# Optimization experiments

Hardware: AMD Instinct MI355X
Metric: run time of the kernel (lower is better)

## Reference

```python
import jax, jax.numpy as jnp
import numpy as np

N = 32768       # total nodes across the batch of graphs
E = 524288      # total edges
D = 512         # feature dim (dimensions = [512, 512, 512])
G = 512         # number of graphs (64 nodes each)


def setup_inputs() -> dict:
    key = jax.random.key(0)
    ks = jax.random.split(key, 16)
    inp = {
        'feat': jax.random.normal(ks[0], (N, D), jnp.float32),
        'src': jax.random.randint(ks[1], (E,), 0, N, jnp.int32),
        'dst': jax.random.randint(ks[2], (E,), 0, N, jnp.int32),
        'adj_vals': jax.random.uniform(ks[3], (E,), jnp.float32),
        'graph_ids': (jnp.arange(N, dtype=jnp.int32) // (N // G)),
        'W0': jax.random.normal(ks[4], (D, D), jnp.float32) * 0.05,
        'b0': jnp.zeros((D,), jnp.float32),
        'W1': jax.random.normal(ks[5], (D, D), jnp.float32) * 0.05,
        'b1': jnp.zeros((D,), jnp.float32),
        'gW1': jax.random.normal(ks[6], (D, D), jnp.float32) * 0.05,
        'gb1': jnp.zeros((D,), jnp.float32),
        'gW2': jax.random.normal(ks[7], (D, D), jnp.float32) * 0.05,
        'gb2': jnp.zeros((D,), jnp.float32),
        'gW3': jax.random.normal(ks[8], (D, D), jnp.float32) * 0.05,
        'gb3': jnp.zeros((D,), jnp.float32),
        'gWs': jax.random.normal(ks[9], (D, D), jnp.float32) * 0.05,
        'gbs': jnp.zeros((D,), jnp.float32),
    }
    return inp


def reference(feat, src, dst, adj_vals, graph_ids,
              W0, b0, W1, b1,
              gW1, gb1, gW2, gb2, gW3, gb3, gWs, gbs):
    # GCN layer: act(A_hat @ (X W) + b), A_hat given as weighted edge list
    def gcn(h, W, b, act):
        support = h @ W                              # [N, D]
        msg = adj_vals[:, None] * support[src]       # [E, D]
        agg = jax.ops.segment_sum(msg, dst, num_segments=N)
        return act(agg + b)

    h = gcn(feat, W0, b0, jax.nn.relu)               # hidden layer, act=relu
    h = gcn(h, W1, b1, lambda x: x)                  # last layer, identity act

    # pooling: per-graph mean readout -> sigmoid -> repeat-expand back to nodes
    ones = jnp.ones((N, 1), h.dtype)
    counts = jax.ops.segment_sum(ones, graph_ids, num_segments=G)   # [G, 1]
    pooled = jax.ops.segment_sum(h, graph_ids, num_segments=G) / counts
    g = jax.nn.sigmoid(pooled)[graph_ids]            # [N, D] repeat-expanded

    z = jax.nn.relu(g @ gW1 + gb1)
    z = jax.nn.relu(z @ gW2 + gb2)
    z = jax.nn.relu(z @ gW3 + gb3)
    return z + (g @ gWs + gbs)
```

## Files before the change

### kernel.cpp

```cpp
#include <hip/hip_runtime.h>

typedef unsigned int u32;
typedef unsigned short u16;

typedef __attribute__((ext_vector_type(8))) __bf16 bf16x8;
typedef __attribute__((ext_vector_type(4))) float f32x4;
typedef __attribute__((ext_vector_type(2))) float f32x2;
typedef __attribute__((ext_vector_type(4))) u32 u32x4;

#define N_NODES 32768
#define N_EDGES 524288
#define DIM 512
#define N_GRAPHS 512
#define ECAP 1536
#define NB_CONV 8192
#define NB_TR 1536

__device__ __forceinline__ u16 f2b(float f) {
  union { float f; u32 u; } v; v.f = f;
  u32 r = v.u + 0x7FFFu + ((v.u >> 16) & 1u);
  return (u16)(r >> 16);
}
__device__ __forceinline__ u32 pack2(float a, float b) {
  return (u32)f2b(a) | ((u32)f2b(b) << 16);
}
__device__ __forceinline__ float blo(u32 u) { union { u32 u; float f; } v; v.u = u << 16; return v.f; }
__device__ __forceinline__ float bhi(u32 u) { union { u32 u; float f; } v; v.u = u & 0xFFFF0000u; return v.f; }
__device__ __forceinline__ float b2f(u16 u) { union { u32 u; float f; } v; v.u = ((u32)u) << 16; return v.f; }

__device__ __forceinline__ void async16(const void* g, void* l) {
  __builtin_amdgcn_global_load_lds(
      (const __attribute__((address_space(1))) u32*)g,
      (__attribute__((address_space(3))) u32*)l, 16, 0, 0);
}

__device__ __forceinline__ void acc8(f32x2* a, u32x4 raw, float v) {
  f32x2 v2 = {v, v};
  a[0] += v2 * f32x2{blo(raw.x), bhi(raw.x)};
  a[1] += v2 * f32x2{blo(raw.y), bhi(raw.y)};
  a[2] += v2 * f32x2{blo(raw.z), bhi(raw.z)};
  a[3] += v2 * f32x2{blo(raw.w), bhi(raw.w)};
}

struct WPack {
  const float* src[6];
  u16* dst[6];
};
__global__ __launch_bounds__(256)
void k_prep(const float* __restrict__ feat, u16* __restrict__ featb, WPack wp,
            const int* __restrict__ dstv, int* __restrict__ counts) {
  __shared__ float tile[32][33];
  const int bid = blockIdx.x, tid = threadIdx.x;
  if (bid < NB_CONV) {
    int i = bid * 256 + tid;
    const float4* p = (const float4*)feat;
    float4 a = p[2 * i], b = p[2 * i + 1];
    uint4 o;
    o.x = pack2(a.x, a.y); o.y = pack2(a.z, a.w);
    o.z = pack2(b.x, b.y); o.w = pack2(b.z, b.w);
    ((uint4*)featb)[i] = o;
  } else if (bid < NB_CONV + NB_TR) {
    int idx = bid - NB_CONV;
    int bz = idx >> 8, rem = idx & 255, by = rem >> 4, bx = rem & 15;
    const float* W = wp.src[bz];
    u16* Wt = wp.dst[bz];
    int tx = tid & 31, ty = tid >> 5;
    int bx32 = bx * 32, by32 = by * 32;
    #pragma unroll
    for (int i = 0; i < 4; i++)
      tile[ty + 8 * i][tx] = W[(size_t)(by32 + ty + 8 * i) * DIM + bx32 + tx];
    __syncthreads();
    #pragma unroll
    for (int i = 0; i < 4; i++)
      Wt[(size_t)(bx32 + ty + 8 * i) * DIM + by32 + tx] = f2b(tile[tx][ty + 8 * i]);
  } else {
    int i = (bid - NB_CONV - NB_TR) * 256 + tid;
    atomicAdd(&counts[dstv[i]], 1);
  }
}

__global__ void k_scan(const int* __restrict__ counts, int* __restrict__ offsets,
                       int* __restrict__ cursor) {
  __shared__ int part[1024];
  int t = threadIdx.x;
  const int4* c4 = (const int4*)counts;
  int4 cv[8];
  #pragma unroll
  for (int j = 0; j < 8; j++) cv[j] = c4[t * 8 + j];
  int loc[32];
  int s = 0;
  #pragma unroll
  for (int j = 0; j < 8; j++) {
    loc[4 * j + 0] = s; s += cv[j].x;
    loc[4 * j + 1] = s; s += cv[j].y;
    loc[4 * j + 2] = s; s += cv[j].z;
    loc[4 * j + 3] = s; s += cv[j].w;
  }
  part[t] = s;
  __syncthreads();
  for (int off = 1; off < 1024; off <<= 1) {
    int v = (t >= off) ? part[t - off] : 0;
    __syncthreads();
    part[t] += v;
    __syncthreads();
  }
  int excl = (t == 0) ? 0 : part[t - 1];
  #pragma unroll
  for (int j = 0; j < 8; j++) {
    int4 o = make_int4(excl + loc[4 * j], excl + loc[4 * j + 1],
                       excl + loc[4 * j + 2], excl + loc[4 * j + 3]);
    ((int4*)offsets)[t * 8 + j] = o;
    ((int4*)cursor)[t * 8 + j] = o;
  }
  if (t == 1023) offsets[N_NODES] = excl + s;
}

__global__ void k_fill(const int* __restrict__ src, const int* __restrict__ dst,
                       const float* __restrict__ vals, int* __restrict__ cursor,
                       int2* __restrict__ epack) {
  int i = blockIdx.x * 256 + threadIdx.x;
  if (i >= N_EDGES) return;
  int d = dst[i];
  int p = atomicAdd(&cursor[d], 1);
  epack[p] = make_int2(src[i], __float_as_int(vals[i]));
}

__global__ __launch_bounds__(256)
void k_gemm_bt(const u16* __restrict__ A, const u16* __restrict__ Bt,
               u16* __restrict__ Cout, int M, int Nout, int K) {
  __shared__ __align__(16) u16 As[128 * 32];
  __shared__ __align__(16) u16 Bs[128 * 32];
  const int tid = threadIdx.x;
  const int l = tid & 63;
  const int w = tid >> 6;
  const int mBase = blockIdx.x * 128;
  const int nBase = blockIdx.y * 128;
  const int wm = (w >> 1) * 64;
  const int wn = (w & 1) * 64;
  const int lrow = l >> 2;
  const int lcol = (l & 3) * 8;
  const int q = l >> 4;
  const int r = l & 15;
  f32x4 acc[4][4] = {};

  for (int k0 = 0; k0 < K; k0 += 32) {
    #pragma unroll
    for (int p = 0; p < 2; p++) {
      int row = w * 32 + p * 16 + lrow;
      async16(A + (size_t)(mBase + row) * K + k0 + lcol, (char*)As + w * 2048 + p * 1024);
      async16(Bt + (size_t)(nBase + row) * K + k0 + lcol, (char*)Bs + w * 2048 + p * 1024);
    }
    __syncthreads();
    bf16x8 af[4], bfr[4];
    #pragma unroll
    for (int i = 0; i < 4; i++) af[i] = *(const bf16x8*)&As[(wm + i * 16 + r) * 32 + q * 8];
    #pragma unroll
    for (int j = 0; j < 4; j++) bfr[j] = *(const bf16x8*)&Bs[(wn + j * 16 + r) * 32 + q * 8];
    #pragma unroll
    for (int i = 0; i < 4; i++)
      #pragma unroll
      for (int j = 0; j < 4; j++)
        acc[i][j] = __builtin_amdgcn_mfma_f32_16x16x32_bf16(af[i], bfr[j], acc[i][j], 0, 0, 0);
    __syncthreads();
  }

  #pragma unroll
  for (int i = 0; i < 4; i++) {
    #pragma unroll
    for (int j = 0; j < 4; j++) {
      int col = nBase + wn + j * 16 + r;
      #pragma unroll
      for (int reg = 0; reg < 4; reg++) {
        int rowg = mBase + wm + i * 16 + q * 4 + reg;
        Cout[(size_t)rowg * Nout + col] = f2b(acc[i][j][reg]);
      }
    }
  }
}

template <bool RELU, bool ADDEND, bool OUTF32, bool SIGMOID>
__global__ __launch_bounds__(256)
void k_gemm_small(const u16* __restrict__ A, const u16* __restrict__ Bt,
                  const float* __restrict__ bias, const u16* __restrict__ addend,
                  void* __restrict__ Cout, int Nout, int K) {
  __shared__ __align__(16) u16 As[64 * 32];
  __shared__ __align__(16) u16 Bs[64 * 32];
  const int tid = threadIdx.x;
  const int l = tid & 63;
  const int w = tid >> 6;
  const int mBase = blockIdx.x * 64;
  const int nBase = blockIdx.y * 64;
  const int wm = (w >> 1) * 32;
  const int wn = (w & 1) * 32;
  const int lrow = tid >> 2;
  const int lcol = (tid & 3) * 8;
  const int q = l >> 4;
  const int r = l & 15;
  f32x4 acc[2][2] = {};

  for (int k0 = 0; k0 < K; k0 += 32) {
    async16(A + (size_t)(mBase + lrow) * K + k0 + lcol, (char*)As + tid * 16);
    async16(Bt + (size_t)(nBase + lrow) * K + k0 + lcol, (char*)Bs + tid * 16);
    __syncthreads();
    bf16x8 af[2], bfr[2];
    #pragma unroll
    for (int i = 0; i < 2; i++) af[i] = *(const bf16x8*)&As[(wm + i * 16 + r) * 32 + q * 8];
    #pragma unroll
    for (int j = 0; j < 2; j++) bfr[j] = *(const bf16x8*)&Bs[(wn + j * 16 + r) * 32 + q * 8];
    #pragma unroll
    for (int i = 0; i < 2; i++)
      #pragma unroll
      for (int j = 0; j < 2; j++)
        acc[i][j] = __builtin_amdgcn_mfma_f32_16x16x32_bf16(af[i], bfr[j], acc[i][j], 0, 0, 0);
    __syncthreads();
  }

  #pragma unroll
  for (int i = 0; i < 2; i++) {
    #pragma unroll
    for (int j = 0; j < 2; j++) {
      int col = nBase + wn + j * 16 + r;
      float bv = bias[col];
      #pragma unroll
      for (int reg = 0; reg < 4; reg++) {
        int rowg = mBase + wm + i * 16 + q * 4 + reg;
        float v = acc[i][j][reg] + bv;
        if (ADDEND) v += b2f(addend[(size_t)rowg * Nout + col]);
        if (RELU) v = fmaxf(v, 0.0f);
        if (SIGMOID) v = 1.0f / (1.0f + expf(-v));
        if (OUTF32) ((float*)Cout)[(size_t)rowg * Nout + col] = v;
        else ((u16*)Cout)[(size_t)rowg * Nout + col] = f2b(v);
      }
    }
  }
}

template <bool RELU, bool POOL>
__global__ __launch_bounds__(256)
void k_agg(const u16* __restrict__ support, const int* __restrict__ offsets,
           const int2* __restrict__ epack, const float* __restrict__ bias,
           u16* __restrict__ outp) {
  __shared__ int2 eLds[ECAP];
  __shared__ float poolLds[4][64];
  const int chunk = blockIdx.x & 7;
  const int cidx  = blockIdx.x >> 3;
  const int rowBase = cidx * 64;
  const int e0b = offsets[rowBase];
  const int nb = offsets[rowBase + 64] - e0b;
  for (int i = threadIdx.x; i < min(nb, ECAP); i += 256)
    eLds[i] = epack[e0b + i];
  __syncthreads();

  const int wi = threadIdx.x >> 6;
  const int l  = threadIdx.x & 63;
  const int grp = l >> 3;
  const int li  = l & 7;
  const int colOff = chunk * 64 + li * 8;
  const u16* spc = support + colOff;

  f32x2 b[4] = {};
  if (!POOL) {
    const float4* bp = (const float4*)(bias + colOff);
    float4 x = bp[0], y = bp[1];
    b[0] = f32x2{x.x, x.y}; b[1] = f32x2{x.z, x.w};
    b[2] = f32x2{y.x, y.y}; b[3] = f32x2{y.z, y.w};
  }

  f32x2 psum[4] = {};

  #pragma unroll
  for (int pass = 0; pass < 2; pass++) {
    int r = rowBase + wi * 16 + pass * 8 + grp;
    int re0 = offsets[r] - e0b;
    int deg = offsets[r + 1] - e0b - re0;

    f32x2 a[4] = {b[0], b[1], b[2], b[3]};

    if (nb <= ECAP) {
      int i = 0;
      for (; i + 4 <= deg; i += 4) {
        int2 p0 = eLds[re0 + i];
        int2 p1 = eLds[re0 + i + 1];
        int2 p2 = eLds[re0 + i + 2];
        int2 p3 = eLds[re0 + i + 3];
        u32x4 r0 = *(const u32x4*)(spc + (size_t)p0.x * DIM);
        u32x4 r1 = *(const u32x4*)(spc + (size_t)p1.x * DIM);
        u32x4 r2 = *(const u32x4*)(spc + (size_t)p2.x * DIM);
        u32x4 r3 = *(const u32x4*)(spc + (size_t)p3.x * DIM);
        acc8(a, r0, __int_as_float(p0.y));
        acc8(a, r1, __int_as_float(p1.y));
        acc8(a, r2, __int_as_float(p2.y));
        acc8(a, r3, __int_as_float(p3.y));
      }
      for (; i < deg; i++) {
        int2 p = eLds[re0 + i];
        u32x4 raw = *(const u32x4*)(spc + (size_t)p.x * DIM);
        acc8(a, raw, __int_as_float(p.y));
      }
    } else {
      for (int i = 0; i < deg; i++) {
        int gi = re0 + i;
        int2 p = (gi < ECAP) ? eLds[gi] : epack[e0b + gi];
        u32x4 raw = *(const u32x4*)(spc + (size_t)p.x * DIM);
        acc8(a, raw, __int_as_float(p.y));
      }
    }

    if (POOL) {
      #pragma unroll
      for (int i = 0; i < 4; i++) psum[i] += a[i];
    } else {
      if (RELU) {
        #pragma unroll
        for (int i = 0; i < 4; i++) {
          a[i].x = fmaxf(a[i].x, 0.0f);
          a[i].y = fmaxf(a[i].y, 0.0f);
        }
      }
      u32x4 o;
      o.x = pack2(a[0].x, a[0].y); o.y = pack2(a[1].x, a[1].y);
      o.z = pack2(a[2].x, a[2].y); o.w = pack2(a[3].x, a[3].y);
      *(u32x4*)(outp + (size_t)r * DIM + colOff) = o;
    }
  }

  if (POOL) {
    #pragma unroll
    for (int k = 0; k < 4; k++) {
      psum[k].x += __shfl_xor(psum[k].x, 8);  psum[k].y += __shfl_xor(psum[k].y, 8);
      psum[k].x += __shfl_xor(psum[k].x, 16); psum[k].y += __shfl_xor(psum[k].y, 16);
      psum[k].x += __shfl_xor(psum[k].x, 32); psum[k].y += __shfl_xor(psum[k].y, 32);
    }
    if (grp == 0) {
      #pragma unroll
      for (int k = 0; k < 4; k++) {
        poolLds[wi][li * 8 + 2 * k]     = psum[k].x;
        poolLds[wi][li * 8 + 2 * k + 1] = psum[k].y;
      }
    }
    __syncthreads();
    if (threadIdx.x < 64) {
      int cc = threadIdx.x;
      float s = poolLds[0][cc] + poolLds[1][cc] + poolLds[2][cc] + poolLds[3][cc];
      outp[(size_t)cidx * DIM + chunk * 64 + cc] = f2b(s * (1.0f / 64.0f));
    }
  }
}

__global__ void k_expand(const float* __restrict__ small, float* __restrict__ out) {
  int i = blockIdx.x * 256 + threadIdx.x;
  int col4 = i & 127;
  int node = i >> 7;
  float4 v = ((const float4*)small)[((node >> 6) << 7) + col4];
  ((float4*)out)[i] = v;
}

extern "C" void kernel_launch(void* const* d_in, const int* in_sizes, int n_in,
                              void* d_out, int out_size, void* d_ws, size_t ws_size,
                              hipStream_t stream) {
  const float* feat = (const float*)d_in[0];
  const int* src    = (const int*)d_in[1];
  const int* dst    = (const int*)d_in[2];
  const float* adj  = (const float*)d_in[3];
  const float* W0  = (const float*)d_in[5];
  const float* b0  = (const float*)d_in[6];
  const float* W1  = (const float*)d_in[7];
  const float* b1  = (const float*)d_in[8];
  const float* gW1 = (const float*)d_in[9];
  const float* gb1 = (const float*)d_in[10];
  const float* gW2 = (const float*)d_in[11];
  const float* gb2 = (const float*)d_in[12];
  const float* gW3 = (const float*)d_in[13];
  const float* gb3 = (const float*)d_in[14];
  const float* gWs = (const float*)d_in[15];
  const float* gbs = (const float*)d_in[16];

  char* ws = (char*)d_ws;
  size_t off = 0;
  auto alloc = [&](size_t bytes) -> void* {
    void* p = ws + off;
    off = (off + bytes + 255) & ~(size_t)255;
    return p;
  };
  u16* bufA = (u16*)alloc((size_t)N_NODES * DIM * 2);
  u16* bufB = (u16*)alloc((size_t)N_NODES * DIM * 2);
  u16* wt[6];
  for (int i = 0; i < 6; i++) wt[i] = (u16*)alloc((size_t)DIM * DIM * 2);
  int* counts   = (int*)alloc((size_t)N_NODES * 4);
  int* offsets  = (int*)alloc((size_t)(N_NODES + 1) * 4);
  int* cursor   = (int*)alloc((size_t)N_NODES * 4);
  int2* epack   = (int2*)alloc((size_t)N_EDGES * 8);
  u16* qb       = (u16*)alloc((size_t)N_GRAPHS * DIM * 2);
  u16* gfeat    = (u16*)alloc((size_t)N_GRAPHS * DIM * 2);
  u16* z1       = (u16*)alloc((size_t)N_GRAPHS * DIM * 2);
  u16* z2       = (u16*)alloc((size_t)N_GRAPHS * DIM * 2);
  u16* z3       = (u16*)alloc((size_t)N_GRAPHS * DIM * 2);
  float* osmall = (float*)alloc((size_t)N_GRAPHS * DIM * 4);

  (void)hipMemsetAsync(counts, 0, (size_t)N_NODES * 4, stream);

  WPack wp;
  wp.src[0] = W0; wp.src[1] = W1; wp.src[2] = gW1; wp.src[3] = gW2; wp.src[4] = gW3; wp.src[5] = gWs;
  for (int i = 0; i < 6; i++) wp.dst[i] = wt[i];

  k_prep<<<NB_CONV + NB_TR + N_EDGES / 256, 256, 0, stream>>>(feat, bufA, wp, dst, counts);
  k_scan<<<1, 1024, 0, stream>>>(counts, offsets, cursor);
  k_fill<<<N_EDGES / 256, 256, 0, stream>>>(src, dst, adj, cursor, epack);

  k_gemm_bt<<<dim3(N_NODES / 128, DIM / 128), 256, 0, stream>>>(bufA, wt[0], bufB, N_NODES, DIM, DIM);
  k_agg<true, false><<<4096, 256, 0, stream>>>(bufB, offsets, epack, b0, bufA);
  k_agg<false, true><<<4096, 256, 0, stream>>>(bufA, offsets, epack, nullptr, qb);
  k_gemm_small<false, false, false, true><<<dim3(8, 8), 256, 0, stream>>>(qb, wt[1], b1, nullptr, gfeat, DIM, DIM);

  k_gemm_small<true, false, false, false><<<dim3(8, 8), 256, 0, stream>>>(gfeat, wt[2], gb1, nullptr, z1, DIM, DIM);
  k_gemm_small<true, false, false, false><<<dim3(8, 8), 256, 0, stream>>>(z1, wt[3], gb2, nullptr, z2, DIM, DIM);
  k_gemm_small<true, false, false, false><<<dim3(8, 8), 256, 0, stream>>>(z2, wt[4], gb3, nullptr, z3, DIM, DIM);
  k_gemm_small<false, true, true, false><<<dim3(8, 8), 256, 0, stream>>>(gfeat, wt[5], gbs, z3, osmall, DIM, DIM);

  k_expand<<<(N_NODES * DIM / 4) / 256, 256, 0, stream>>>(osmall, (float*)d_out);
}
```

Before: 391.9 us.

## Balance pooled aggregation across threads by edge ranges instead of rows

The pooling aggregation kernel now splits each 64-node group's edges evenly across 32 thread slots, ignoring row boundaries, since only the per-graph sum is needed. This removes the load imbalance from per-row degree variance and unrolls the gather eight edges deep for more memory-level parallelism. Edge records held in LDS are padded to avoid bank conflicts, with a smaller LDS cap and a fallback to global memory. The fill kernel also packs the low destination bits into the source index, which the readers mask off. Blocks whose edge count exceeds the smaller cap read edges straight from global memory.

```diff
diff --git a/kernel.cpp b/kernel.cpp
--- a/kernel.cpp
+++ b/kernel.cpp
@@ -12,7 +12,9 @@
 #define N_EDGES 524288
 #define DIM 512
 #define N_GRAPHS 512
-#define ECAP 1536
+#define ECAP_ROW 1536
+#define ECAP 1216
+#define ELDS_SZ (ECAP + ECAP / 32 + 1)
 #define NB_CONV 8192
 #define NB_TR 1536
 
@@ -33,6 +35,8 @@
       (const __attribute__((address_space(1))) u32*)g,
       (__attribute__((address_space(3))) u32*)l, 16, 0, 0);
 }
+
+__device__ __forceinline__ int eidx(int i) { return i + (i >> 5); }
 
 __device__ __forceinline__ void acc8(f32x2* a, u32x4 raw, float v) {
   f32x2 v2 = {v, v};
@@ -122,7 +126,7 @@
   if (i >= N_EDGES) return;
   int d = dst[i];
   int p = atomicAdd(&cursor[d], 1);
-  epack[p] = make_int2(src[i], __float_as_int(vals[i]));
+  epack[p] = make_int2(src[i] | ((d & 63) << 15), __float_as_int(vals[i]));
 }
 
 __global__ __launch_bounds__(256)
@@ -235,19 +239,17 @@
   }
 }
 
-template <bool RELU, bool POOL>
 __global__ __launch_bounds__(256)
-void k_agg(const u16* __restrict__ support, const int* __restrict__ offsets,
-           const int2* __restrict__ epack, const float* __restrict__ bias,
-           u16* __restrict__ outp) {
-  __shared__ int2 eLds[ECAP];
-  __shared__ float poolLds[4][64];
+void k_agg_row(const u16* __restrict__ support, const int* __restrict__ offsets,
+               const int2* __restrict__ epack, const float* __restrict__ bias,
+               u16* __restrict__ outp) {
+  __shared__ int2 eLds[ECAP_ROW];
   const int chunk = blockIdx.x & 7;
   const int cidx  = blockIdx.x >> 3;
   const int rowBase = cidx * 64;
   const int e0b = offsets[rowBase];
   const int nb = offsets[rowBase + 64] - e0b;
-  for (int i = threadIdx.x; i < min(nb, ECAP); i += 256)
+  for (int i = threadIdx.x; i < min(nb, ECAP_ROW); i += 256)
     eLds[i] = epack[e0b + i];
   __syncthreads();
 
@@ -258,16 +260,14 @@
   const int colOff = chunk * 64 + li * 8;
   const u16* spc = support + colOff;
 
-  f32x2 b[4] = {};
-  if (!POOL) {
+  f32x2 b[4];
+  {
     const float4* bp = (const float4*)(bias + colOff);
     float4 x = bp[0], y = bp[1];
     b[0] = f32x2{x.x, x.y}; b[1] = f32x2{x.z, x.w};
     b[2] = f32x2{y.x, y.y}; b[3] = f32x2{y.z, y.w};
   }
 
-  f32x2 psum[4] = {};
-
   #pragma unroll
   for (int pass = 0; pass < 2; pass++) {
     int r = rowBase + wi * 16 + pass * 8 + grp;
@@ -276,17 +276,17 @@
 
     f32x2 a[4] = {b[0], b[1], b[2], b[3]};
 
-    if (nb <= ECAP) {
+    if (nb <= ECAP_ROW) {
       int i = 0;
       for (; i + 4 <= deg; i += 4) {
         int2 p0 = eLds[re0 + i];
         int2 p1 = eLds[re0 + i + 1];
         int2 p2 = eLds[re0 + i + 2];
         int2 p3 = eLds[re0 + i + 3];
-        u32x4 r0 = *(const u32x4*)(spc + (size_t)p0.x * DIM);
-        u32x4 r1 = *(const u32x4*)(spc + (size_t)p1.x * DIM);
-        u32x4 r2 = *(const u32x4*)(spc + (size_t)p2.x * DIM);
-        u32x4 r3 = *(const u32x4*)(spc + (size_t)p3.x * DIM);
+        u32x4 r0 = *(const u32x4*)(spc + (size_t)(p0.x & 32767) * DIM);
+        u32x4 r1 = *(const u32x4*)(spc + (size_t)(p1.x & 32767) * DIM);
+        u32x4 r2 = *(const u32x4*)(spc + (size_t)(p2.x & 32767) * DIM);
+        u32x4 r3 = *(const u32x4*)(spc + (size_t)(p3.x & 32767) * DIM);
         acc8(a, r0, __int_as_float(p0.y));
         acc8(a, r1, __int_as_float(p1.y));
         acc8(a, r2, __int_as_float(p2.y));
@@ -294,56 +294,111 @@
       }
       for (; i < deg; i++) {
         int2 p = eLds[re0 + i];
-        u32x4 raw = *(const u32x4*)(spc + (size_t)p.x * DIM);
+        u32x4 raw = *(const u32x4*)(spc + (size_t)(p.x & 32767) * DIM);
         acc8(a, raw, __int_as_float(p.y));
       }
     } else {
       for (int i = 0; i < deg; i++) {
         int gi = re0 + i;
-        int2 p = (gi < ECAP) ? eLds[gi] : epack[e0b + gi];
-        u32x4 raw = *(const u32x4*)(spc + (size_t)p.x * DIM);
+        int2 p = (gi < ECAP_ROW) ? eLds[gi] : epack[e0b + gi];
+        u32x4 raw = *(const u32x4*)(spc + (size_t)(p.x & 32767) * DIM);
         acc8(a, raw, __int_as_float(p.y));
       }
     }
 
-    if (POOL) {
-      #pragma unroll
-      for (int i = 0; i < 4; i++) psum[i] += a[i];
-    } else {
-      if (RELU) {
-        #pragma unroll
-        for (int i = 0; i < 4; i++) {
-          a[i].x = fmaxf(a[i].x, 0.0f);
-          a[i].y = fmaxf(a[i].y, 0.0f);
-        }
-      }
-      u32x4 o;
-      o.x = pack2(a[0].x, a[0].y); o.y = pack2(a[1].x, a[1].y);
-      o.z = pack2(a[2].x, a[2].y); o.w = pack2(a[3].x, a[3].y);
-      *(u32x4*)(outp + (size_t)r * DIM + colOff) = o;
-    }
-  }
-
-  if (POOL) {
+    #pragma unroll
+    for (int i = 0; i < 4; i++) {
+      a[i].x = fmaxf(a[i].x, 0.0f);
+      a[i].y = fmaxf(a[i].y, 0.0f);
+    }
+    u32x4 o;
+    o.x = pack2(a[0].x, a[0].y); o.y = pack2(a[1].x, a[1].y);
+    o.z = pack2(a[2].x, a[2].y); o.w = pack2(a[3].x, a[3].y);
+    *(u32x4*)(outp + (size_t)r * DIM + colOff) = o;
+  }
+}
+
+__global__ __launch_bounds__(256)
+void k_agg_pool(const u16* __restrict__ support, const int* __restrict__ offsets,
+                const int2* __restrict__ epack, u16* __restrict__ outp) {
+  __shared__ int2 eLds[ELDS_SZ];
+  __shared__ float redLds[256];
+
+  const int tid = threadIdx.x;
+  const int chunk = blockIdx.x & 7;
+  const int cidx = blockIdx.x >> 3;
+  const int rowBase = cidx * 64;
+  const int e0b = offsets[rowBase];
+  const int nb = offsets[rowBase + 64] - e0b;
+  const bool fits = (nb <= ECAP);
+
+  if (fits) {
+    for (int i = tid; i < nb; i += 256) eLds[eidx(i)] = epack[e0b + i];
+  }
+  __syncthreads();
+
+  const int slot = tid >> 3;
+  const int li = tid & 7;
+  const int colOff = chunk * 64 + li * 8;
+  const u16* spc = support + colOff;
+  const int e0 = (nb * slot) >> 5;
+  const int e1 = (nb * (slot + 1)) >> 5;
+
+  f32x2 psum[4] = {};
+
+  auto consume = [&](int2 p, u32x4 rw) {
+    float v = __int_as_float(p.y);
+    f32x2 v2 = {v, v};
+    psum[0] += v2 * f32x2{blo(rw.x), bhi(rw.x)};
+    psum[1] += v2 * f32x2{blo(rw.y), bhi(rw.y)};
+    psum[2] += v2 * f32x2{blo(rw.z), bhi(rw.z)};
+    psum[3] += v2 * f32x2{blo(rw.w), bhi(rw.w)};
+  };
+
+  if (fits) {
+    int i = e0;
+    for (; i + 8 <= e1; i += 8) {
+      int2 p[8];
+      #pragma unroll
+      for (int j = 0; j < 8; j++) p[j] = eLds[eidx(i + j)];
+      u32x4 rw[8];
+      #pragma unroll
+      for (int j = 0; j < 8; j++)
+        rw[j] = *(const u32x4*)(spc + (size_t)(p[j].x & 32767) * DIM);
+      #pragma unroll
+      for (int j = 0; j < 8; j++) consume(p[j], rw[j]);
+    }
+    for (; i < e1; i++) {
+      int2 p = eLds[eidx(i)];
+      u32x4 rw = *(const u32x4*)(spc + (size_t)(p.x & 32767) * DIM);
+      consume(p, rw);
+    }
+  } else {
+    for (int i = e0; i < e1; i++) {
+      int2 p = epack[e0b + i];
+      u32x4 rw = *(const u32x4*)(spc + (size_t)(p.x & 32767) * DIM);
+      consume(p, rw);
+    }
+  }
+
+  #pragma unroll
+  for (int k = 0; k < 4; k++) {
+    psum[k].x += __shfl_xor(psum[k].x, 8);  psum[k].y += __shfl_xor(psum[k].y, 8);
+    psum[k].x += __shfl_xor(psum[k].x, 16); psum[k].y += __shfl_xor(psum[k].y, 16);
+    psum[k].x += __shfl_xor(psum[k].x, 32); psum[k].y += __shfl_xor(psum[k].y, 32);
+  }
+  const int wi = tid >> 6;
+  if (((tid >> 3) & 7) == 0) {
     #pragma unroll
     for (int k = 0; k < 4; k++) {
-      psum[k].x += __shfl_xor(psum[k].x, 8);  psum[k].y += __shfl_xor(psum[k].y, 8);
-      psum[k].x += __shfl_xor(psum[k].x, 16); psum[k].y += __shfl_xor(psum[k].y, 16);
-      psum[k].x += __shfl_xor(psum[k].x, 32); psum[k].y += __shfl_xor(psum[k].y, 32);
-    }
-    if (grp == 0) {
-      #pragma unroll
-      for (int k = 0; k < 4; k++) {
-        poolLds[wi][li * 8 + 2 * k]     = psum[k].x;
-        poolLds[wi][li * 8 + 2 * k + 1] = psum[k].y;
-      }
-    }
-    __syncthreads();
-    if (threadIdx.x < 64) {
-      int cc = threadIdx.x;
-      float s = poolLds[0][cc] + poolLds[1][cc] + poolLds[2][cc] + poolLds[3][cc];
-      outp[(size_t)cidx * DIM + chunk * 64 + cc] = f2b(s * (1.0f / 64.0f));
-    }
+      redLds[wi * 64 + li * 8 + 2 * k]     = psum[k].x;
+      redLds[wi * 64 + li * 8 + 2 * k + 1] = psum[k].y;
+    }
+  }
+  __syncthreads();
+  if (tid < 64) {
+    float s = redLds[tid] + redLds[64 + tid] + redLds[128 + tid] + redLds[192 + tid];
+    outp[(size_t)cidx * DIM + chunk * 64 + tid] = f2b(s * (1.0f / 64.0f));
   }
 }
 
@@ -408,8 +463,8 @@
   k_fill<<<N_EDGES / 256, 256, 0, stream>>>(src, dst, adj, cursor, epack);
 
   k_gemm_bt<<<dim3(N_NODES / 128, DIM / 128), 256, 0, stream>>>(bufA, wt[0], bufB, N_NODES, DIM, DIM);
-  k_agg<true, false><<<4096, 256, 0, stream>>>(bufB, offsets, epack, b0, bufA);
-  k_agg<false, true><<<4096, 256, 0, stream>>>(bufA, offsets, epack, nullptr, qb);
+  k_agg_row<<<4096, 256, 0, stream>>>(bufB, offsets, epack, b0, bufA);
+  k_agg_pool<<<4096, 256, 0, stream>>>(bufA, offsets, epack, qb);
   k_gemm_small<false, false, false, true><<<dim3(8, 8), 256, 0, stream>>>(qb, wt[1], b1, nullptr, gfeat, DIM, DIM);
 
   k_gemm_small<true, false, false, false><<<dim3(8, 8), 256, 0, stream>>>(gfeat, wt[2], gb1, nullptr, z1, DIM, DIM);
```

Measured after the change: 384.2 us. 2.0% less time.
